# Optimization experiments

Hardware: AMD Instinct MI355X
Metric: run time of the kernel (lower is better)

## Reference

```python
import jax, jax.numpy as jnp
import numpy as np

N_SRC, N_TGT, K, L, C_OUT = 16384, 16384, 16, 128, 2
E = N_TGT * K
MIN_VAR = 1e-3   # adf.keep_variance_fn min variance (applied in Dropout)
DROP_P = 0.2
INV_SQRT2 = np.float32(1.0 / np.sqrt(2.0))
INV_SQRT2PI = np.float32(1.0 / np.sqrt(2.0 * np.pi))


def setup_inputs() -> dict:
    key = jax.random.key(0)
    ks = jax.random.split(key, 12)
    pos_source = jax.random.uniform(ks[0], (N_SRC, 3), jnp.float32)
    pos_target = jax.random.uniform(ks[1], (N_TGT, 3), jnp.float32)
    latents = jax.random.normal(ks[2], (N_SRC, L), jnp.float32)
    var = jax.random.uniform(ks[3], (N_SRC, L), jnp.float32)
    # KNN-style edge list: each target has K source neighbors
    row = jnp.repeat(jnp.arange(N_TGT, dtype=jnp.int32), K)          # [E] target idx
    col = jax.random.randint(ks[4], (E,), 0, N_SRC, jnp.int32)       # [E] source idx
    occupancies = jax.random.randint(ks[5], (N_TGT,), 0, 2, jnp.int32)
    # fixed inverted-dropout mask (deterministic stand-in for adf.Dropout training mask)
    drop_mask = (jax.random.uniform(ks[6], (E, L)) >= DROP_P).astype(jnp.float32) / (1.0 - DROP_P)
    def init_w(k, sh):
        return jax.random.normal(k, sh, jnp.float32) * np.float32(1.0 / np.sqrt(sh[-1]))
    W_in = init_w(ks[7], (L, L + 3)); b_in = jnp.zeros((L,), jnp.float32)
    W1 = init_w(ks[8], (L, L)); b1 = jnp.zeros((L,), jnp.float32)
    W2 = init_w(ks[9], (L, L)); b2 = jnp.zeros((L,), jnp.float32)
    W_out = init_w(ks[10], (C_OUT, L)); b_out = jnp.zeros((C_OUT,), jnp.float32)
    return dict(pos_source=pos_source, pos_target=pos_target, latents=latents, var=var,
                drop_mask=drop_mask, W_in=W_in, b_in=b_in, W1=W1, b1=b1, W2=W2, b2=b2,
                W_out=W_out, b_out=b_out, row=row, col=col, occupancies=occupancies)


def _adf_linear(m, v, W, b):
    # ADF Linear: mean -> affine; variance -> through squared weights, no bias
    return m @ W.T + b, v @ (W * W).T


def _adf_relu(m, v):
    # ADF ReLU moment matching (Gast & Roth); clamp var for sqrt stability
    v = jnp.maximum(v, 1e-6)
    std = jnp.sqrt(v)
    r = m / std
    cdf = 0.5 * (1.0 + jax.lax.erf(r * INV_SQRT2))
    pdf = jnp.exp(-0.5 * r * r) * INV_SQRT2PI
    m_out = m * cdf + std * pdf
    v_out = (m * m + v) * cdf + m * std * pdf - m_out * m_out
    return m_out, v_out


def reference(pos_source, pos_target, latents, var, drop_mask, W_in, b_in, W1, b1, W2, b2, W_out, b_out, row, col, occupancies):
    pos_rel = pos_target[row] - pos_source[col]                    # [E,3]
    m = jnp.concatenate([latents[col], pos_rel], axis=1)           # [E,L+3]
    v = jnp.concatenate([var[col], pos_rel], axis=1)               # [E,L+3] (faithful: pos_rel reused as 'variance')
    m, v = _adf_linear(m, v, W_in, b_in)
    for W, b in ((W1, b1), (W2, b2)):
        m, v = _adf_relu(m, v)
        m, v = _adf_linear(m, v, W, b)
    # ADF dropout with keep_variance_fn
    m = m * drop_mask
    v = v * drop_mask * drop_mask + MIN_VAR
    m, v = _adf_linear(m, v, W_out, b_out)                         # [E,2]
    preds = m[:, 0]
    aleatoric = jnp.abs(v[:, 0]).mean()
    occ_gt = occupancies[row].astype(jnp.float32)
    # stable binary_cross_entropy_with_logits, mean reduction
    recons_loss = jnp.mean(jnp.maximum(preds, 0.0) - preds * occ_gt + jnp.log1p(jnp.exp(-jnp.abs(preds))))
    return preds, aleatoric, recons_loss, occ_gt
```

## Files before the change

kernel.cpp:

```cpp
#include <hip/hip_runtime.h>
#include <math.h>

#define E_TOT 262144
#define LDIM  128
#define XPB   272
#define MIN_VARF 0.001f
#define INV_SQRT2PIF 0.3989422804014327f
#define NBLK  (E_TOT / 64)

typedef _Float16 half8 __attribute__((ext_vector_type(8)));
typedef float    f32x4 __attribute__((ext_vector_type(4)));
typedef float    f32x2 __attribute__((ext_vector_type(2)));

#define BIAS_OFF  256
#define WOUT_OFF  1792
#define BOUT_OFF  2816
#define PK_L0     4096
#define PK_L1     45056
#define PK_L2     77824
#define PART_OFF  110592

__device__ __forceinline__ short h2s(float x) {
    union U { _Float16 h; short s; } u; u.h = (_Float16)x; return u.s;
}

__device__ __forceinline__ void adf_relu(float& m, float& v) {
    float vv = fmaxf(v, 1e-6f);
    float is = __builtin_amdgcn_rsqf(vv);
    float sd = vv * is;
    float r  = m * is;
    float qq = 0.5f * r * r;
    float sp = sd * __expf(-qq) * INV_SQRT2PIF;
    const float A = 0.147f;
    float aq  = A * qq;
    float num = qq * (1.27323954f + aq);
    float den = 1.0f + aq;
    float z   = -num * __builtin_amdgcn_rcpf(den);
    float wv  = 1.0f - __expf(z);
    float s   = wv * __builtin_amdgcn_rsqf(fmaxf(wv, 1e-20f));
    float serf = copysignf(s, m);
    float cdf  = 0.5f + 0.5f * serf;
    float mo = fmaf(m, cdf, sp);
    float vo = fmaf(fmaf(m, m, vv), cdf, fmaf(m, sp, -mo * mo));
    m = mo; v = vo;
}

__global__ void prep(const float* __restrict__ W_in, const float* __restrict__ b_in,
                     const float* __restrict__ W1,   const float* __restrict__ b1,
                     const float* __restrict__ W2,   const float* __restrict__ b2,
                     const float* __restrict__ W_out,const float* __restrict__ b_out,
                     char* __restrict__ ws)
{
    int idx = blockIdx.x * 256 + threadIdx.x;
    if (idx < 6656) {
        const float* W; int Kfull; long dstoff; int entry;
        if (idx < 2560)      { entry = idx;        W = W_in; Kfull = 131; dstoff = PK_L0; }
        else if (idx < 4608) { entry = idx - 2560; W = W1;   Kfull = 128; dstoff = PK_L1; }
        else                 { entry = idx - 4608; W = W2;   Kfull = 128; dstoff = PK_L2; }
        int ks   = entry >> 9;
        int rest = entry & 511;
        int t    = rest >> 6;
        int lane = rest & 63;
        int rowi = t * 16 + (lane & 15);
        int k0   = ks * 32 + (lane >> 4) * 8;
        half8 hv;
#pragma unroll
        for (int j = 0; j < 8; ++j) {
            int k = k0 + j;
            hv[j] = (_Float16)((k < Kfull) ? W[rowi * Kfull + k] : 0.0f);
        }
        *(half8*)(ws + dstoff + (long)entry * 16) = hv;
    } else if (idx < 6656 + 384) {
        int j = idx - 6656; int layer = j >> 7; int pidx = j & 127;
        int gg = pidx >> 5, t = (pidx >> 2) & 7, r = pidx & 3;
        int n = t * 16 + gg * 4 + r;
        const float* b = layer == 0 ? b_in : (layer == 1 ? b1 : b2);
        ((float*)(ws + BIAS_OFF))[layer * 128 + pidx] = b[n];
    } else if (idx < 6656 + 384 + 256) {
        int j = idx - 6656 - 384; int path = j >> 7; int pidx = j & 127;
        int gg = pidx >> 5, t = (pidx >> 2) & 7, r = pidx & 3;
        int n = t * 16 + gg * 4 + r;
        float v = W_out[n];
        if (path) v = v * v;
        ((float*)(ws + WOUT_OFF))[path * 128 + pidx] = v;
    } else if (idx == 6656 + 384 + 256) {
        ((float*)(ws + BOUT_OFF))[0] = b_out[0];
    }
}

__global__ void __launch_bounds__(256, 3)
interp_main(const float* __restrict__ pos_source, const float* __restrict__ pos_target,
            const float* __restrict__ latents,    const float* __restrict__ varr,
            const float* __restrict__ drop_mask,
            const int* __restrict__ row, const int* __restrict__ col, const int* __restrict__ occ,
            float* __restrict__ out, char* __restrict__ ws)
{
    __shared__ __align__(16) short Xm[64][XPB / 2];
    __shared__ __align__(16) short Xv[64][XPB / 2];
    __shared__ float wred[4][2];

    const int tid  = threadIdx.x;
    const int lane = tid & 63;
    const int w    = tid >> 6;
    const int q    = lane & 15;
    const int g    = lane >> 4;
    const int erow = w * 16 + q;
    const int gbase = blockIdx.x * 64;
    const int ge   = gbase + erow;
    char* xmb = (char*)&Xm[0][0];
    char* xvb = (char*)&Xv[0][0];

    f32x4 md[8];
    {
        const f32x4* dmp = (const f32x4*)drop_mask + (size_t)ge * 32 + g;
#pragma unroll
        for (int t = 0; t < 8; ++t) md[t] = __builtin_nontemporal_load(dmp + t * 4);
    }
    const int c0 = col[ge];
    const int r0 = row[ge];
    const float occf = (float)occ[r0];
    const float px = pos_target[r0 * 3 + 0] - pos_source[c0 * 3 + 0];
    const float py = pos_target[r0 * 3 + 1] - pos_source[c0 * 3 + 1];
    const float pz = pos_target[r0 * 3 + 2] - pos_source[c0 * 3 + 2];

    half8 bm4[4], bv4[4];
    {
        const float* lm = latents + (long)c0 * LDIM;
        const float* lv = varr    + (long)c0 * LDIM;
#pragma unroll
        for (int ks = 0; ks < 4; ++ks) {
            const f32x4* am4 = (const f32x4*)(lm + ks * 32 + g * 8);
            const f32x4* av4 = (const f32x4*)(lv + ks * 32 + g * 8);
            f32x4 fm0 = am4[0], fm1 = am4[1];
            f32x4 fv0 = av4[0], fv1 = av4[1];
            half8 bm, bv;
#pragma unroll
            for (int j = 0; j < 4; ++j) {
                bm[j] = (_Float16)fm0[j]; bm[j + 4] = (_Float16)fm1[j];
                bv[j] = (_Float16)fv0[j]; bv[j + 4] = (_Float16)fv1[j];
            }
            bm4[ks] = bm; bv4[ks] = bv;
        }
    }

    f32x4 accm[8], accv[8];
    const f32x4 zz = {0.0f, 0.0f, 0.0f, 0.0f};
#pragma unroll
    for (int t = 0; t < 8; ++t) { accm[t] = zz; accv[t] = zz; }

    {
        const char* pk = ws + PK_L0 + lane * 16;
#pragma unroll
        for (int ks = 0; ks < 4; ++ks) {
            const char* pmk = pk + ks * 8192;
            half8 bm = bm4[ks], bv = bv4[ks];
#pragma unroll
            for (int t = 0; t < 8; ++t) {
                half8 am = *(const half8*)(pmk + t * 1024);
                half8 av = am * am;
                accm[t] = __builtin_amdgcn_mfma_f32_16x16x32_f16(am, bm, accm[t], 0, 0, 0);
                accv[t] = __builtin_amdgcn_mfma_f32_16x16x32_f16(av, bv, accv[t], 0, 0, 0);
            }
        }
        half8 bpos = {(_Float16)0.f, (_Float16)0.f, (_Float16)0.f, (_Float16)0.f,
                      (_Float16)0.f, (_Float16)0.f, (_Float16)0.f, (_Float16)0.f};
        if (g == 0) { bpos[0] = (_Float16)px; bpos[1] = (_Float16)py; bpos[2] = (_Float16)pz; }
        const char* pmk = pk + 4 * 8192;
#pragma unroll
        for (int t = 0; t < 8; ++t) {
            half8 am = *(const half8*)(pmk + t * 1024);
            half8 av = am * am;
            accm[t] = __builtin_amdgcn_mfma_f32_16x16x32_f16(am, bpos, accm[t], 0, 0, 0);
            accv[t] = __builtin_amdgcn_mfma_f32_16x16x32_f16(av, bpos, accv[t], 0, 0, 0);
        }
        const f32x4* bp = (const f32x4*)(ws + BIAS_OFF) + g * 8;
#pragma unroll
        for (int t = 0; t < 8; ++t) {
            f32x4 b4 = bp[t];
            float m0 = accm[t][0] + b4[0], m1 = accm[t][1] + b4[1];
            float m2 = accm[t][2] + b4[2], m3 = accm[t][3] + b4[3];
            float v0 = accv[t][0], v1 = accv[t][1], v2 = accv[t][2], v3 = accv[t][3];
            adf_relu(m0, v0); adf_relu(m1, v1); adf_relu(m2, v2); adf_relu(m3, v3);
            short4 sm; sm.x = h2s(m0); sm.y = h2s(m1); sm.z = h2s(m2); sm.w = h2s(m3);
            short4 sv; sv.x = h2s(v0); sv.y = h2s(v1); sv.z = h2s(v2); sv.w = h2s(v3);
            *(short4*)(xmb + erow * XPB + t * 32 + g * 8) = sm;
            *(short4*)(xvb + erow * XPB + t * 32 + g * 8) = sv;
        }
    }

#pragma unroll
    for (int t = 0; t < 8; ++t) { accm[t] = zz; accv[t] = zz; }
    {
        const char* pk = ws + PK_L1 + lane * 16;
#pragma unroll
        for (int ks = 0; ks < 4; ++ks) {
            half8 bm = *(const half8*)(xmb + erow * XPB + ks * 64 + g * 16);
            half8 bv = *(const half8*)(xvb + erow * XPB + ks * 64 + g * 16);
            const char* pmk = pk + ks * 8192;
#pragma unroll
            for (int t = 0; t < 8; ++t) {
                half8 am = *(const half8*)(pmk + t * 1024);
                half8 av = am * am;
                accm[t] = __builtin_amdgcn_mfma_f32_16x16x32_f16(am, bm, accm[t], 0, 0, 0);
                accv[t] = __builtin_amdgcn_mfma_f32_16x16x32_f16(av, bv, accv[t], 0, 0, 0);
            }
        }
        const f32x4* bp = (const f32x4*)(ws + BIAS_OFF) + 32 + g * 8;
#pragma unroll
        for (int t = 0; t < 8; ++t) {
            f32x4 b4 = bp[t];
            float m0 = accm[t][0] + b4[0], m1 = accm[t][1] + b4[1];
            float m2 = accm[t][2] + b4[2], m3 = accm[t][3] + b4[3];
            float v0 = accv[t][0], v1 = accv[t][1], v2 = accv[t][2], v3 = accv[t][3];
            adf_relu(m0, v0); adf_relu(m1, v1); adf_relu(m2, v2); adf_relu(m3, v3);
            short4 sm; sm.x = h2s(m0); sm.y = h2s(m1); sm.z = h2s(m2); sm.w = h2s(m3);
            short4 sv; sv.x = h2s(v0); sv.y = h2s(v1); sv.z = h2s(v2); sv.w = h2s(v3);
            *(short4*)(xmb + erow * XPB + t * 32 + g * 8) = sm;
            *(short4*)(xvb + erow * XPB + t * 32 + g * 8) = sv;
        }
    }

#pragma unroll
    for (int t = 0; t < 8; ++t) { accm[t] = zz; accv[t] = zz; }
    {
        const char* pk = ws + PK_L2 + lane * 16;
#pragma unroll
        for (int ks = 0; ks < 4; ++ks) {
            half8 bm = *(const half8*)(xmb + erow * XPB + ks * 64 + g * 16);
            half8 bv = *(const half8*)(xvb + erow * XPB + ks * 64 + g * 16);
            const char* pmk = pk + ks * 8192;
#pragma unroll
            for (int t = 0; t < 8; ++t) {
                half8 am = *(const half8*)(pmk + t * 1024);
                half8 av = am * am;
                accm[t] = __builtin_amdgcn_mfma_f32_16x16x32_f16(am, bm, accm[t], 0, 0, 0);
                accv[t] = __builtin_amdgcn_mfma_f32_16x16x32_f16(av, bv, accv[t], 0, 0, 0);
            }
        }
    }

    {
        float pmacc = 0.0f, pvacc = 0.0f;
        const f32x4* wmp = (const f32x4*)(ws + WOUT_OFF);
        const f32x4* bp  = (const f32x4*)(ws + BIAS_OFF) + 64 + g * 8;
#pragma unroll
        for (int t = 0; t < 8; ++t) {
            f32x4 b4 = bp[t];
            f32x4 d4 = md[t];
            f32x4 w4 = wmp[g * 8 + t];
            f32x4 s4 = wmp[32 + g * 8 + t];
            float m0 = (accm[t][0] + b4[0]) * d4[0];
            float m1 = (accm[t][1] + b4[1]) * d4[1];
            float m2 = (accm[t][2] + b4[2]) * d4[2];
            float m3 = (accm[t][3] + b4[3]) * d4[3];
            float v0 = accv[t][0] * d4[0] * d4[0] + MIN_VARF;
            float v1 = accv[t][1] * d4[1] * d4[1] + MIN_VARF;
            float v2 = accv[t][2] * d4[2] * d4[2] + MIN_VARF;
            float v3 = accv[t][3] * d4[3] * d4[3] + MIN_VARF;
            pmacc += w4[0] * m0 + w4[1] * m1 + w4[2] * m2 + w4[3] * m3;
            pvacc += s4[0] * v0 + s4[1] * v1 + s4[2] * v2 + s4[3] * v3;
        }
        pmacc += __shfl_xor(pmacc, 16, 64);
        pmacc += __shfl_xor(pmacc, 32, 64);
        pvacc += __shfl_xor(pvacc, 16, 64);
        pvacc += __shfl_xor(pvacc, 32, 64);
        float bout = *(const float*)(ws + BOUT_OFF);
        float p = pmacc + bout;
        if (lane < 16) {
            out[ge] = p;
            out[E_TOT + 2 + ge] = occf;
        }
        float a = fabsf(p);
        float loss = fmaxf(p, 0.0f) - p * occf + __logf(1.0f + __expf(-a));
        float al = fabsf(pvacc);
#pragma unroll
        for (int off = 1; off < 16; off <<= 1) {
            al   += __shfl_xor(al, off, 64);
            loss += __shfl_xor(loss, off, 64);
        }
        if (lane == 0) { wred[w][0] = al; wred[w][1] = loss; }
    }
    __syncthreads();
    if (tid == 0) {
        f32x2 s;
        s[0] = wred[0][0] + wred[1][0] + wred[2][0] + wred[3][0];
        s[1] = wred[0][1] + wred[1][1] + wred[2][1] + wred[3][1];
        *((f32x2*)(ws + PART_OFF) + blockIdx.x) = s;
    }
}

__global__ void __launch_bounds__(256)
interp_finalize(const char* __restrict__ ws, float* __restrict__ out)
{
    __shared__ float sal[4], sls[4];
    const int tid  = threadIdx.x;
    const int lane = tid & 63;
    const int w    = tid >> 6;
    float al = 0.0f, ls = 0.0f;
    const f32x2* part = (const f32x2*)(ws + PART_OFF);
    for (int i = tid; i < NBLK; i += 256) {
        f32x2 p = part[i];
        al += p[0]; ls += p[1];
    }
#pragma unroll
    for (int off = 1; off < 64; off <<= 1) {
        al += __shfl_xor(al, off, 64);
        ls += __shfl_xor(ls, off, 64);
    }
    if (lane == 0) { sal[w] = al; sls[w] = ls; }
    __syncthreads();
    if (tid == 0) {
        const float inv = 1.0f / (float)E_TOT;
        out[E_TOT]     = (sal[0] + sal[1] + sal[2] + sal[3]) * inv;
        out[E_TOT + 1] = (sls[0] + sls[1] + sls[2] + sls[3]) * inv;
    }
}

extern "C" void kernel_launch(void* const* d_in, const int* in_sizes, int n_in,
                              void* d_out, int out_size, void* d_ws, size_t ws_size,
                              hipStream_t stream) {
    (void)in_sizes; (void)n_in; (void)out_size; (void)ws_size;
    const float* pos_source = (const float*)d_in[0];
    const float* pos_target = (const float*)d_in[1];
    const float* latents    = (const float*)d_in[2];
    const float* varr       = (const float*)d_in[3];
    const float* drop_mask  = (const float*)d_in[4];
    const float* W_in       = (const float*)d_in[5];
    const float* b_in       = (const float*)d_in[6];
    const float* W1         = (const float*)d_in[7];
    const float* b1         = (const float*)d_in[8];
    const float* W2         = (const float*)d_in[9];
    const float* b2         = (const float*)d_in[10];
    const float* W_out      = (const float*)d_in[11];
    const float* b_out      = (const float*)d_in[12];
    const int*   row        = (const int*)d_in[13];
    const int*   col        = (const int*)d_in[14];
    const int*   occ        = (const int*)d_in[15];
    float* out = (float*)d_out;
    char*  ws  = (char*)d_ws;

    prep<<<29, 256, 0, stream>>>(W_in, b_in, W1, b1, W2, b2, W_out, b_out, ws);
    interp_main<<<NBLK, 256, 0, stream>>>(
        pos_source, pos_target, latents, varr, drop_mask,
        row, col, occ, out, ws);
    interp_finalize<<<1, 256, 0, stream>>>(ws, out);
}
```

Before: 156.5 us.

## Process two edge tiles per wave to reuse weight fragments across MFMAs

Each block now handles 128 edges instead of 64, with each wave computing two 16-edge tiles that share every loaded weight fragment and its squared copy, halving weight loads and squaring per MFMA. The erf approximation inside ADF ReLU is replaced by an Abramowitz-Stegun polynomial that reuses the exp already computed for the pdf, which drops one exp and one rsqrt. Float-to-half conversion now uses packed round-toward-zero conversion, and the dropout mask is loaded late, in the epilogue, instead of being held in registers. The cost is doubled accumulator registers, occupancy lowered to 2 blocks per CU, more LDS per block, and half as many blocks.

```diff
diff --git a/kernel.cpp b/kernel.cpp
--- a/kernel.cpp
+++ b/kernel.cpp
@@ -6,11 +6,14 @@
 #define XPB   272
 #define MIN_VARF 0.001f
 #define INV_SQRT2PIF 0.3989422804014327f
-#define NBLK  (E_TOT / 64)
-
-typedef _Float16 half8 __attribute__((ext_vector_type(8)));
-typedef float    f32x4 __attribute__((ext_vector_type(4)));
-typedef float    f32x2 __attribute__((ext_vector_type(2)));
+#define EPB   128
+#define NBLK  (E_TOT / EPB)
+
+typedef _Float16 half8  __attribute__((ext_vector_type(8)));
+typedef __fp16   fp16x2 __attribute__((ext_vector_type(2)));
+typedef float    f32x4  __attribute__((ext_vector_type(4)));
+typedef float    f32x2  __attribute__((ext_vector_type(2)));
+typedef unsigned int uint2v __attribute__((ext_vector_type(2)));
 
 #define BIAS_OFF  256
 #define WOUT_OFF  1792
@@ -20,8 +23,16 @@
 #define PK_L2     77824
 #define PART_OFF  110592
 
-__device__ __forceinline__ short h2s(float x) {
-    union U { _Float16 h; short s; } u; u.h = (_Float16)x; return u.s;
+__device__ __forceinline__ unsigned int pkrtz(float a, float b) {
+    union { fp16x2 h; unsigned int u; } z;
+    z.h = __builtin_amdgcn_cvt_pkrtz(a, b);
+    return z.u;
+}
+__device__ __forceinline__ half8 to_h8(f32x4 a, f32x4 b) {
+    union { half8 h; unsigned int u[4]; } z;
+    z.u[0] = pkrtz(a[0], a[1]); z.u[1] = pkrtz(a[2], a[3]);
+    z.u[2] = pkrtz(b[0], b[1]); z.u[3] = pkrtz(b[2], b[3]);
+    return z.h;
 }
 
 __device__ __forceinline__ void adf_relu(float& m, float& v) {
@@ -30,16 +41,14 @@
     float sd = vv * is;
     float r  = m * is;
     float qq = 0.5f * r * r;
-    float sp = sd * __expf(-qq) * INV_SQRT2PIF;
-    const float A = 0.147f;
-    float aq  = A * qq;
-    float num = qq * (1.27323954f + aq);
-    float den = 1.0f + aq;
-    float z   = -num * __builtin_amdgcn_rcpf(den);
-    float wv  = 1.0f - __expf(z);
-    float s   = wv * __builtin_amdgcn_rsqf(fmaxf(wv, 1e-20f));
-    float serf = copysignf(s, m);
-    float cdf  = 0.5f + 0.5f * serf;
+    float e  = __expf(-qq);
+    float sp = sd * e * INV_SQRT2PIF;
+    const float P = 0.23165247f;
+    float t  = __builtin_amdgcn_rcpf(fmaf(fabsf(r), P, 1.0f));
+    float poly = t * fmaf(t, fmaf(t, fmaf(t, fmaf(t, 1.061405429f, -1.453152027f),
+                                          1.421413741f), -0.284496736f), 0.254829592f);
+    float erfa = fmaf(-poly, e, 1.0f);
+    float cdf  = fmaf(copysignf(0.5f, r), erfa, 0.5f);
     float mo = fmaf(m, cdf, sp);
     float vo = fmaf(fmaf(m, m, vv), cdf, fmaf(m, sp, -mo * mo));
     m = mo; v = vo;
@@ -88,15 +97,32 @@
     }
 }
 
-__global__ void __launch_bounds__(256, 3)
+__device__ __forceinline__ void epi_store(const f32x4* am, const f32x4* av, const f32x4* bp,
+                                          char* xmb, char* xvb, int rowb, int g8)
+{
+#pragma unroll
+    for (int t = 0; t < 8; ++t) {
+        f32x4 b4 = bp[t];
+        float m0 = am[t][0] + b4[0], m1 = am[t][1] + b4[1];
+        float m2 = am[t][2] + b4[2], m3 = am[t][3] + b4[3];
+        float v0 = av[t][0], v1 = av[t][1], v2 = av[t][2], v3 = av[t][3];
+        adf_relu(m0, v0); adf_relu(m1, v1); adf_relu(m2, v2); adf_relu(m3, v3);
+        uint2v sm = {pkrtz(m0, m1), pkrtz(m2, m3)};
+        uint2v sv = {pkrtz(v0, v1), pkrtz(v2, v3)};
+        *(uint2v*)(xmb + rowb + t * 32 + g8) = sm;
+        *(uint2v*)(xvb + rowb + t * 32 + g8) = sv;
+    }
+}
+
+__global__ void __launch_bounds__(256, 2)
 interp_main(const float* __restrict__ pos_source, const float* __restrict__ pos_target,
             const float* __restrict__ latents,    const float* __restrict__ varr,
             const float* __restrict__ drop_mask,
             const int* __restrict__ row, const int* __restrict__ col, const int* __restrict__ occ,
             float* __restrict__ out, char* __restrict__ ws)
 {
-    __shared__ __align__(16) short Xm[64][XPB / 2];
-    __shared__ __align__(16) short Xv[64][XPB / 2];
+    __shared__ __align__(16) short Xm[EPB][XPB / 2];
+    __shared__ __align__(16) short Xv[EPB][XPB / 2];
     __shared__ float wred[4][2];
 
     const int tid  = threadIdx.x;
@@ -104,175 +130,146 @@
     const int w    = tid >> 6;
     const int q    = lane & 15;
     const int g    = lane >> 4;
-    const int erow = w * 16 + q;
-    const int gbase = blockIdx.x * 64;
-    const int ge   = gbase + erow;
+    const int g8   = g * 8;
+    const int er0  = w * 32 + q;
+    const int er1  = er0 + 16;
+    const int ge0  = blockIdx.x * EPB + er0;
+    const int ge1  = ge0 + 16;
     char* xmb = (char*)&Xm[0][0];
     char* xvb = (char*)&Xv[0][0];
 
-    f32x4 md[8];
+    const int c0 = col[ge0], c1 = col[ge1];
+    const int r0 = row[ge0], r1 = row[ge1];
+    const float occf0 = (float)occ[r0];
+    const float occf1 = (float)occ[r1];
+    const float px0 = pos_target[r0 * 3 + 0] - pos_source[c0 * 3 + 0];
+    const float py0 = pos_target[r0 * 3 + 1] - pos_source[c0 * 3 + 1];
+    const float pz0 = pos_target[r0 * 3 + 2] - pos_source[c0 * 3 + 2];
+    const float px1 = pos_target[r1 * 3 + 0] - pos_source[c1 * 3 + 0];
+    const float py1 = pos_target[r1 * 3 + 1] - pos_source[c1 * 3 + 1];
+    const float pz1 = pos_target[r1 * 3 + 2] - pos_source[c1 * 3 + 2];
+
+    f32x4 acm0[8], acv0[8], acm1[8], acv1[8];
+    const f32x4 zz = {0.0f, 0.0f, 0.0f, 0.0f};
+#pragma unroll
+    for (int t = 0; t < 8; ++t) { acm0[t] = zz; acv0[t] = zz; acm1[t] = zz; acv1[t] = zz; }
+
     {
-        const f32x4* dmp = (const f32x4*)drop_mask + (size_t)ge * 32 + g;
-#pragma unroll
-        for (int t = 0; t < 8; ++t) md[t] = __builtin_nontemporal_load(dmp + t * 4);
-    }
-    const int c0 = col[ge];
-    const int r0 = row[ge];
-    const float occf = (float)occ[r0];
-    const float px = pos_target[r0 * 3 + 0] - pos_source[c0 * 3 + 0];
-    const float py = pos_target[r0 * 3 + 1] - pos_source[c0 * 3 + 1];
-    const float pz = pos_target[r0 * 3 + 2] - pos_source[c0 * 3 + 2];
-
-    half8 bm4[4], bv4[4];
-    {
-        const float* lm = latents + (long)c0 * LDIM;
-        const float* lv = varr    + (long)c0 * LDIM;
+        const char*  pk  = ws + PK_L0 + lane * 16;
+        const float* lm0 = latents + (long)c0 * LDIM;
+        const float* lv0 = varr    + (long)c0 * LDIM;
+        const float* lm1 = latents + (long)c1 * LDIM;
+        const float* lv1 = varr    + (long)c1 * LDIM;
 #pragma unroll
         for (int ks = 0; ks < 4; ++ks) {
-            const f32x4* am4 = (const f32x4*)(lm + ks * 32 + g * 8);
-            const f32x4* av4 = (const f32x4*)(lv + ks * 32 + g * 8);
-            f32x4 fm0 = am4[0], fm1 = am4[1];
-            f32x4 fv0 = av4[0], fv1 = av4[1];
-            half8 bm, bv;
-#pragma unroll
-            for (int j = 0; j < 4; ++j) {
-                bm[j] = (_Float16)fm0[j]; bm[j + 4] = (_Float16)fm1[j];
-                bv[j] = (_Float16)fv0[j]; bv[j + 4] = (_Float16)fv1[j];
-            }
-            bm4[ks] = bm; bv4[ks] = bv;
-        }
-    }
-
-    f32x4 accm[8], accv[8];
-    const f32x4 zz = {0.0f, 0.0f, 0.0f, 0.0f};
-#pragma unroll
-    for (int t = 0; t < 8; ++t) { accm[t] = zz; accv[t] = zz; }
-
-    {
-        const char* pk = ws + PK_L0 + lane * 16;
-#pragma unroll
-        for (int ks = 0; ks < 4; ++ks) {
+            const f32x4* a0 = (const f32x4*)(lm0 + ks * 32 + g8);
+            const f32x4* s0 = (const f32x4*)(lv0 + ks * 32 + g8);
+            const f32x4* a1 = (const f32x4*)(lm1 + ks * 32 + g8);
+            const f32x4* s1 = (const f32x4*)(lv1 + ks * 32 + g8);
+            half8 bm0 = to_h8(a0[0], a0[1]);
+            half8 bv0 = to_h8(s0[0], s0[1]);
+            half8 bm1 = to_h8(a1[0], a1[1]);
+            half8 bv1 = to_h8(s1[0], s1[1]);
             const char* pmk = pk + ks * 8192;
-            half8 bm = bm4[ks], bv = bv4[ks];
 #pragma unroll
             for (int t = 0; t < 8; ++t) {
                 half8 am = *(const half8*)(pmk + t * 1024);
                 half8 av = am * am;
-                accm[t] = __builtin_amdgcn_mfma_f32_16x16x32_f16(am, bm, accm[t], 0, 0, 0);
-                accv[t] = __builtin_amdgcn_mfma_f32_16x16x32_f16(av, bv, accv[t], 0, 0, 0);
+                acm0[t] = __builtin_amdgcn_mfma_f32_16x16x32_f16(am, bm0, acm0[t], 0, 0, 0);
+                acm1[t] = __builtin_amdgcn_mfma_f32_16x16x32_f16(am, bm1, acm1[t], 0, 0, 0);
+                acv0[t] = __builtin_amdgcn_mfma_f32_16x16x32_f16(av, bv0, acv0[t], 0, 0, 0);
+                acv1[t] = __builtin_amdgcn_mfma_f32_16x16x32_f16(av, bv1, acv1[t], 0, 0, 0);
             }
         }
-        half8 bpos = {(_Float16)0.f, (_Float16)0.f, (_Float16)0.f, (_Float16)0.f,
-                      (_Float16)0.f, (_Float16)0.f, (_Float16)0.f, (_Float16)0.f};
-        if (g == 0) { bpos[0] = (_Float16)px; bpos[1] = (_Float16)py; bpos[2] = (_Float16)pz; }
+        half8 bp0 = {(_Float16)0.f, (_Float16)0.f, (_Float16)0.f, (_Float16)0.f,
+                     (_Float16)0.f, (_Float16)0.f, (_Float16)0.f, (_Float16)0.f};
+        half8 bp1 = bp0;
+        if (g == 0) {
+            bp0[0] = (_Float16)px0; bp0[1] = (_Float16)py0; bp0[2] = (_Float16)pz0;
+            bp1[0] = (_Float16)px1; bp1[1] = (_Float16)py1; bp1[2] = (_Float16)pz1;
+        }
         const char* pmk = pk + 4 * 8192;
 #pragma unroll
         for (int t = 0; t < 8; ++t) {
             half8 am = *(const half8*)(pmk + t * 1024);
             half8 av = am * am;
-            accm[t] = __builtin_amdgcn_mfma_f32_16x16x32_f16(am, bpos, accm[t], 0, 0, 0);
-            accv[t] = __builtin_amdgcn_mfma_f32_16x16x32_f16(av, bpos, accv[t], 0, 0, 0);
+            acm0[t] = __builtin_amdgcn_mfma_f32_16x16x32_f16(am, bp0, acm0[t], 0, 0, 0);
+            acm1[t] = __builtin_amdgcn_mfma_f32_16x16x32_f16(am, bp1, acm1[t], 0, 0, 0);
+            acv0[t] = __builtin_amdgcn_mfma_f32_16x16x32_f16(av, bp0, acv0[t], 0, 0, 0);
+            acv1[t] = __builtin_amdgcn_mfma_f32_16x16x32_f16(av, bp1, acv1[t], 0, 0, 0);
         }
         const f32x4* bp = (const f32x4*)(ws + BIAS_OFF) + g * 8;
-#pragma unroll
-        for (int t = 0; t < 8; ++t) {
-            f32x4 b4 = bp[t];
-            float m0 = accm[t][0] + b4[0], m1 = accm[t][1] + b4[1];
-            float m2 = accm[t][2] + b4[2], m3 = accm[t][3] + b4[3];
-            float v0 = accv[t][0], v1 = accv[t][1], v2 = accv[t][2], v3 = accv[t][3];
-            adf_relu(m0, v0); adf_relu(m1, v1); adf_relu(m2, v2); adf_relu(m3, v3);
-            short4 sm; sm.x = h2s(m0); sm.y = h2s(m1); sm.z = h2s(m2); sm.w = h2s(m3);
-            short4 sv; sv.x = h2s(v0); sv.y = h2s(v1); sv.z = h2s(v2); sv.w = h2s(v3);
-            *(short4*)(xmb + erow * XPB + t * 32 + g * 8) = sm;
-            *(short4*)(xvb + erow * XPB + t * 32 + g * 8) = sv;
-        }
-    }
-
-#pragma unroll
-    for (int t = 0; t < 8; ++t) { accm[t] = zz; accv[t] = zz; }
-    {
-        const char* pk = ws + PK_L1 + lane * 16;
+        epi_store(acm0, acv0, bp, xmb, xvb, er0 * XPB, g8);
+        epi_store(acm1, acv1, bp, xmb, xvb, er1 * XPB, g8);
+    }
+
+    for (int layer = 1; layer < 3; ++layer) {
+        const char* pk = ws + (layer == 1 ? PK_L1 : PK_L2) + lane * 16;
+#pragma unroll
+        for (int t = 0; t < 8; ++t) { acm0[t] = zz; acv0[t] = zz; acm1[t] = zz; acv1[t] = zz; }
 #pragma unroll
         for (int ks = 0; ks < 4; ++ks) {
-            half8 bm = *(const half8*)(xmb + erow * XPB + ks * 64 + g * 16);
-            half8 bv = *(const half8*)(xvb + erow * XPB + ks * 64 + g * 16);
+            half8 bm0 = *(const half8*)(xmb + er0 * XPB + ks * 64 + g * 16);
+            half8 bv0 = *(const half8*)(xvb + er0 * XPB + ks * 64 + g * 16);
+            half8 bm1 = *(const half8*)(xmb + er1 * XPB + ks * 64 + g * 16);
+            half8 bv1 = *(const half8*)(xvb + er1 * XPB + ks * 64 + g * 16);
             const char* pmk = pk + ks * 8192;
 #pragma unroll
             for (int t = 0; t < 8; ++t) {
                 half8 am = *(const half8*)(pmk + t * 1024);
                 half8 av = am * am;
-                accm[t] = __builtin_amdgcn_mfma_f32_16x16x32_f16(am, bm, accm[t], 0, 0, 0);
-                accv[t] = __builtin_amdgcn_mfma_f32_16x16x32_f16(av, bv, accv[t], 0, 0, 0);
+                acm0[t] = __builtin_amdgcn_mfma_f32_16x16x32_f16(am, bm0, acm0[t], 0, 0, 0);
+                acm1[t] = __builtin_amdgcn_mfma_f32_16x16x32_f16(am, bm1, acm1[t], 0, 0, 0);
+                acv0[t] = __builtin_amdgcn_mfma_f32_16x16x32_f16(av, bv0, acv0[t], 0, 0, 0);
+                acv1[t] = __builtin_amdgcn_mfma_f32_16x16x32_f16(av, bv1, acv1[t], 0, 0, 0);
             }
         }
-        const f32x4* bp = (const f32x4*)(ws + BIAS_OFF) + 32 + g * 8;
+        if (layer == 1) {
+            const f32x4* bp = (const f32x4*)(ws + BIAS_OFF) + 32 + g * 8;
+            epi_store(acm0, acv0, bp, xmb, xvb, er0 * XPB, g8);
+            epi_store(acm1, acv1, bp, xmb, xvb, er1 * XPB, g8);
+        }
+    }
+
+    {
+        const f32x4* wmp = (const f32x4*)(ws + WOUT_OFF);
+        const f32x4* bp  = (const f32x4*)(ws + BIAS_OFF) + 64 + g * 8;
+        const f32x4* dm0 = (const f32x4*)(drop_mask + (size_t)ge0 * LDIM) + g;
+        const f32x4* dm1 = (const f32x4*)(drop_mask + (size_t)ge1 * LDIM) + g;
+        float pm0 = 0.f, pv0 = 0.f, pm1 = 0.f, pv1 = 0.f;
 #pragma unroll
         for (int t = 0; t < 8; ++t) {
             f32x4 b4 = bp[t];
-            float m0 = accm[t][0] + b4[0], m1 = accm[t][1] + b4[1];
-            float m2 = accm[t][2] + b4[2], m3 = accm[t][3] + b4[3];
-            float v0 = accv[t][0], v1 = accv[t][1], v2 = accv[t][2], v3 = accv[t][3];
-            adf_relu(m0, v0); adf_relu(m1, v1); adf_relu(m2, v2); adf_relu(m3, v3);
-            short4 sm; sm.x = h2s(m0); sm.y = h2s(m1); sm.z = h2s(m2); sm.w = h2s(m3);
-            short4 sv; sv.x = h2s(v0); sv.y = h2s(v1); sv.z = h2s(v2); sv.w = h2s(v3);
-            *(short4*)(xmb + erow * XPB + t * 32 + g * 8) = sm;
-            *(short4*)(xvb + erow * XPB + t * 32 + g * 8) = sv;
-        }
-    }
-
-#pragma unroll
-    for (int t = 0; t < 8; ++t) { accm[t] = zz; accv[t] = zz; }
-    {
-        const char* pk = ws + PK_L2 + lane * 16;
-#pragma unroll
-        for (int ks = 0; ks < 4; ++ks) {
-            half8 bm = *(const half8*)(xmb + erow * XPB + ks * 64 + g * 16);
-            half8 bv = *(const half8*)(xvb + erow * XPB + ks * 64 + g * 16);
-            const char* pmk = pk + ks * 8192;
-#pragma unroll
-            for (int t = 0; t < 8; ++t) {
-                half8 am = *(const half8*)(pmk + t * 1024);
-                half8 av = am * am;
-                accm[t] = __builtin_amdgcn_mfma_f32_16x16x32_f16(am, bm, accm[t], 0, 0, 0);
-                accv[t] = __builtin_amdgcn_mfma_f32_16x16x32_f16(av, bv, accv[t], 0, 0, 0);
-            }
-        }
-    }
-
-    {
-        float pmacc = 0.0f, pvacc = 0.0f;
-        const f32x4* wmp = (const f32x4*)(ws + WOUT_OFF);
-        const f32x4* bp  = (const f32x4*)(ws + BIAS_OFF) + 64 + g * 8;
-#pragma unroll
-        for (int t = 0; t < 8; ++t) {
-            f32x4 b4 = bp[t];
-            f32x4 d4 = md[t];
             f32x4 w4 = wmp[g * 8 + t];
             f32x4 s4 = wmp[32 + g * 8 + t];
-            float m0 = (accm[t][0] + b4[0]) * d4[0];
-            float m1 = (accm[t][1] + b4[1]) * d4[1];
-            float m2 = (accm[t][2] + b4[2]) * d4[2];
-            float m3 = (accm[t][3] + b4[3]) * d4[3];
-            float v0 = accv[t][0] * d4[0] * d4[0] + MIN_VARF;
-            float v1 = accv[t][1] * d4[1] * d4[1] + MIN_VARF;
-            float v2 = accv[t][2] * d4[2] * d4[2] + MIN_VARF;
-            float v3 = accv[t][3] * d4[3] * d4[3] + MIN_VARF;
-            pmacc += w4[0] * m0 + w4[1] * m1 + w4[2] * m2 + w4[3] * m3;
-            pvacc += s4[0] * v0 + s4[1] * v1 + s4[2] * v2 + s4[3] * v3;
-        }
-        pmacc += __shfl_xor(pmacc, 16, 64);
-        pmacc += __shfl_xor(pmacc, 32, 64);
-        pvacc += __shfl_xor(pvacc, 16, 64);
-        pvacc += __shfl_xor(pvacc, 32, 64);
+            f32x4 d0 = __builtin_nontemporal_load(dm0 + t * 4);
+            f32x4 d1 = __builtin_nontemporal_load(dm1 + t * 4);
+#pragma unroll
+            for (int j = 0; j < 4; ++j) {
+                float m0 = (acm0[t][j] + b4[j]) * d0[j];
+                float v0 = acv0[t][j] * d0[j] * d0[j] + MIN_VARF;
+                float m1 = (acm1[t][j] + b4[j]) * d1[j];
+                float v1 = acv1[t][j] * d1[j] * d1[j] + MIN_VARF;
+                pm0 = fmaf(w4[j], m0, pm0); pv0 = fmaf(s4[j], v0, pv0);
+                pm1 = fmaf(w4[j], m1, pm1); pv1 = fmaf(s4[j], v1, pv1);
+            }
+        }
+        pm0 += __shfl_xor(pm0, 16, 64); pm0 += __shfl_xor(pm0, 32, 64);
+        pv0 += __shfl_xor(pv0, 16, 64); pv0 += __shfl_xor(pv0, 32, 64);
+        pm1 += __shfl_xor(pm1, 16, 64); pm1 += __shfl_xor(pm1, 32, 64);
+        pv1 += __shfl_xor(pv1, 16, 64); pv1 += __shfl_xor(pv1, 32, 64);
         float bout = *(const float*)(ws + BOUT_OFF);
-        float p = pmacc + bout;
+        float p0 = pm0 + bout;
+        float p1 = pm1 + bout;
         if (lane < 16) {
-            out[ge] = p;
-            out[E_TOT + 2 + ge] = occf;
-        }
-        float a = fabsf(p);
-        float loss = fmaxf(p, 0.0f) - p * occf + __logf(1.0f + __expf(-a));
-        float al = fabsf(pvacc);
+            out[ge0] = p0;            out[ge1] = p1;
+            out[E_TOT + 2 + ge0] = occf0;
+            out[E_TOT + 2 + ge1] = occf1;
+        }
+        float a0 = fabsf(p0), a1 = fabsf(p1);
+        float loss = fmaxf(p0, 0.f) - p0 * occf0 + __logf(1.0f + __expf(-a0))
+                   + fmaxf(p1, 0.f) - p1 * occf1 + __logf(1.0f + __expf(-a1));
+        float al = fabsf(pv0) + fabsf(pv1);
 #pragma unroll
         for (int off = 1; off < 16; off <<= 1) {
             al   += __shfl_xor(al, off, 64);
```

Measured after the change: 158.1 us. No clear change (+1.0%).
